# Performance work log

Measured on AMD Instinct MI355X. Metric: run time of the kernel, lower is better.

## Reference

```python
import jax, jax.numpy as jnp
import numpy as np

HEAD_DIM = 128
ROPE_THETA = 10000.0


def _rope_cos_sin(positions, head_dim, theta):
    # positions: [T] int -> cos/sin [T, head_dim] (LLaMA half-split convention)
    inv_freq = 1.0 / (theta ** (jnp.arange(0, head_dim, 2, dtype=jnp.float32) / head_dim))
    ang = positions.astype(jnp.float32)[:, None] * inv_freq  # [T, D/2]
    cos = jnp.concatenate([jnp.cos(ang), jnp.cos(ang)], axis=-1)
    sin = jnp.concatenate([jnp.sin(ang), jnp.sin(ang)], axis=-1)
    return cos, sin


def _apply_rope(x, cos, sin):
    # x: [T, H, D]; rotate_half: (-x2, x1)
    half = x.shape[-1] // 2
    rot = jnp.concatenate([-x[..., half:], x[..., :half]], axis=-1)
    return x * cos[:, None, :] + rot * sin[:, None, :]


def setup_inputs() -> dict:
    key = jax.random.key(0)
    ks = jax.random.split(key, 5)
    T, hid = 4096, 4096
    S = 1024  # equal-length sequences -> B = T // S = 4
    Hq, Hk, D = 32, 8, HEAD_DIM
    hidden = jax.random.normal(ks[0], (T, hid), dtype=jnp.float32)
    positions = (jnp.arange(T, dtype=jnp.int32) % S)
    q_w = jax.random.normal(ks[1], (Hq * D, hid), dtype=jnp.float32) * 0.02
    k_w = jax.random.normal(ks[2], (Hk * D, hid), dtype=jnp.float32) * 0.02
    v_w = jax.random.normal(ks[3], (Hk * D, hid), dtype=jnp.float32) * 0.02
    o_w = jax.random.normal(ks[4], (hid, Hq * D), dtype=jnp.float32) * 0.02
    return {"hidden": hidden, "positions": positions, "q_w": q_w, "k_w": k_w,
            "v_w": v_w, "o_w": o_w, "seq_len": S}


def reference(hidden, positions, q_w, k_w, v_w, o_w, seq_len):
    T, hid = hidden.shape
    D = HEAD_DIM
    Hq = q_w.shape[0] // D
    Hk = k_w.shape[0] // D
    G = Hq // Hk  # num_kv_groups
    S = int(seq_len)
    B = T // S
    # QKV projections (ColumnParallel, tp=1): y = x @ W^T
    q = (hidden @ q_w.T).reshape(T, Hq, D)
    k = (hidden @ k_w.T).reshape(T, Hk, D)
    v = (hidden @ v_w.T).reshape(T, Hk, D)
    # fused RoPE on q and k
    cos, sin = _rope_cos_sin(positions, D, ROPE_THETA)
    q = _apply_rope(q, cos, sin)
    k = _apply_rope(k, cos, sin)
    # varlen (equal-length) causal GQA attention
    q = q.reshape(B, S, Hk, G, D)
    k = k.reshape(B, S, Hk, D)
    v = v.reshape(B, S, Hk, D)
    scale = 1.0 / np.sqrt(D).astype(np.float32)
    scores = jnp.einsum('bqhgd,bkhd->bhgqk', q, k) * scale  # [B,Hk,G,S,S]
    causal = jnp.tril(jnp.ones((S, S), dtype=bool))
    scores = jnp.where(causal, scores, jnp.asarray(-1e30, scores.dtype))
    attn = jax.nn.softmax(scores, axis=-1)
    out = jnp.einsum('bhgqk,bkhd->bqhgd', attn, v).reshape(T, Hq * D)
    # output projection (RowParallel, tp=1)
    return out @ o_w.T
```

## Files before the change

kernel.cpp:

```cpp
#include <hip/hip_runtime.h>
#include <hip/hip_bf16.h>

typedef __attribute__((ext_vector_type(8))) short bf16x8;
typedef __attribute__((ext_vector_type(4))) float f32x4;
typedef __attribute__((ext_vector_type(8))) unsigned short u16x8;

__device__ inline unsigned short f2bf(float f) {
  unsigned u = __builtin_bit_cast(unsigned, f);
  u += 0x7FFFu + ((u >> 16) & 1u);
  return (unsigned short)(u >> 16);
}
__device__ inline float b2f(unsigned short h) {
  unsigned u = ((unsigned)h) << 16;
  return __builtin_bit_cast(float, u);
}

typedef const __attribute__((address_space(1))) void* gas_ptr;
typedef __attribute__((address_space(3))) void* las_ptr;
__device__ inline void load_lds16(const void* g, void* l) {
  __builtin_amdgcn_global_load_lds((gas_ptr)g, (las_ptr)l, 16, 0, 0);
}

#define PHB() do { asm volatile("" ::: "memory"); __builtin_amdgcn_s_barrier(); \
                   __builtin_amdgcn_sched_barrier(0); } while (0)
#define PHB_MID() do { asm volatile("" ::: "memory"); __builtin_amdgcn_s_barrier(); } while (0)

__global__ __launch_bounds__(256) void cvt_f32_bf16(const float* __restrict__ src,
                                                    unsigned short* __restrict__ dst,
                                                    int n4) {
  int i = blockIdx.x * 256 + threadIdx.x;
  if (i >= n4) return;
  float4 v = ((const float4*)src)[i];
  ushort4 o;
  o.x = f2bf(v.x); o.y = f2bf(v.y); o.z = f2bf(v.z); o.w = f2bf(v.w);
  ((ushort4*)dst)[i] = o;
}

__device__ inline void stage_half(const unsigned short* __restrict__ g, int ld,
                                  size_t grow0, int kcol0, char* ldsdst, int tid) {
#pragma unroll
  for (int i = 0; i < 2; ++i) {
    int c = tid + i * 512;
    int r = c >> 3;
    int k = (c & 7) ^ (r & 7);
    load_lds16(g + (grow0 + r) * ld + kcol0 + k * 8, ldsdst + c * 16);
  }
}

template <bool OUT_F32>
__global__ __launch_bounds__(512, 2) void gemm8(const unsigned short* __restrict__ A,
                                                const unsigned short* __restrict__ B,
                                                void* __restrict__ Cv,
                                                int M, int N, int K) {
  __shared__ __attribute__((aligned(16))) char lds[131072];
  const int tid = threadIdx.x;
  const int wave = tid >> 6, lane = tid & 63;
  const int l15 = lane & 15, l4 = lane >> 4, swz = l15 & 7;
  const int wr = wave >> 2, wc = wave & 3;
  const int nTN = N >> 8;
  const int cpx = gridDim.x >> 3;
  const int orig = blockIdx.x;
  const int wg = (orig & 7) * cpx + (orig >> 3);
  const int bm = wg / nTN, bn = wg % nTN;
  const size_t rowA0 = (size_t)bm << 8, rowB0 = (size_t)bn << 8;
  const int nt = K >> 6;
  const int brow = (wc & 1) * 64;

  stage_half(A, K, rowA0,       0,  lds + 0,             tid);
  stage_half(A, K, rowA0 + 128, 0,  lds + 16384,         tid);
  stage_half(B, K, rowB0,       0,  lds + 32768,         tid);
  stage_half(B, K, rowB0 + 128, 0,  lds + 49152,         tid);
  stage_half(A, K, rowA0,       64, lds + 65536,         tid);
  stage_half(A, K, rowA0 + 128, 64, lds + 65536 + 16384, tid);
  stage_half(B, K, rowB0,       64, lds + 65536 + 32768, tid);
  stage_half(B, K, rowB0 + 128, 64, lds + 65536 + 49152, tid);
  asm volatile("s_waitcnt vmcnt(8)" ::: "memory");
  __builtin_amdgcn_s_barrier();
  __builtin_amdgcn_sched_barrier(0);

  f32x4 acc[8][4] = {};
  bf16x8 bf01[2][2];

  {
    const char* bufB0 = lds + 32768 + (wc >> 1) * 16384;
#pragma unroll
    for (int n = 0; n < 2; ++n)
#pragma unroll
      for (int kk = 0; kk < 2; ++kk)
        bf01[n][kk] = *(const bf16x8*)(bufB0 + ((brow + n * 16 + l15) << 7) + (((kk * 4 + l4) ^ swz) << 4));
  }

#pragma unroll 2
  for (int t = 0; t < nt; ++t) {
    char* cbuf = lds + (t & 1) * 65536;
    char* obuf = lds + ((t + 1) & 1) * 65536;
    const char* bufA = cbuf + wr * 16384;
    const char* bufB = cbuf + 32768 + (wc >> 1) * 16384;
    const int kc2 = (t + 2) << 6;

    bf16x8 af[8][2], bf23[2][2];

#pragma unroll
    for (int m = 0; m < 4; ++m)
#pragma unroll
      for (int kk = 0; kk < 2; ++kk)
        af[m][kk] = *(const bf16x8*)(bufA + ((m * 16 + l15) << 7) + (((kk * 4 + l4) ^ swz) << 4));
    PHB_MID();
    __builtin_amdgcn_s_setprio(1);
#pragma unroll
    for (int m = 0; m < 4; ++m)
#pragma unroll
      for (int n = 0; n < 2; ++n)
#pragma unroll
        for (int kk = 0; kk < 2; ++kk)
          acc[m][n] = __builtin_amdgcn_mfma_f32_16x16x32_bf16(af[m][kk], bf01[n][kk], acc[m][n], 0, 0, 0);
    __builtin_amdgcn_s_setprio(0);
    PHB();

#pragma unroll
    for (int n = 0; n < 2; ++n)
#pragma unroll
      for (int kk = 0; kk < 2; ++kk)
        bf23[n][kk] = *(const bf16x8*)(bufB + ((brow + (n + 2) * 16 + l15) << 7) + (((kk * 4 + l4) ^ swz) << 4));
    PHB_MID();
    __builtin_amdgcn_s_setprio(1);
#pragma unroll
    for (int m = 0; m < 4; ++m)
#pragma unroll
      for (int n = 0; n < 2; ++n)
#pragma unroll
        for (int kk = 0; kk < 2; ++kk)
          acc[m][n + 2] = __builtin_amdgcn_mfma_f32_16x16x32_bf16(af[m][kk], bf23[n][kk], acc[m][n + 2], 0, 0, 0);
    __builtin_amdgcn_s_setprio(0);
    PHB();

#pragma unroll
    for (int m = 4; m < 8; ++m)
#pragma unroll
      for (int kk = 0; kk < 2; ++kk)
        af[m][kk] = *(const bf16x8*)(bufA + ((m * 16 + l15) << 7) + (((kk * 4 + l4) ^ swz) << 4));
    if (t < nt - 2) {
      stage_half(B, K, rowB0,       kc2, cbuf + 32768, tid);
      stage_half(B, K, rowB0 + 128, kc2, cbuf + 49152, tid);
    }
    PHB_MID();
    __builtin_amdgcn_s_setprio(1);
#pragma unroll
    for (int m = 4; m < 8; ++m)
#pragma unroll
      for (int n = 0; n < 2; ++n)
#pragma unroll
        for (int kk = 0; kk < 2; ++kk)
          acc[m][n] = __builtin_amdgcn_mfma_f32_16x16x32_bf16(af[m][kk], bf01[n][kk], acc[m][n], 0, 0, 0);
    __builtin_amdgcn_s_setprio(0);
    PHB();

    if (t < nt - 2) {
      stage_half(A, K, rowA0,       kc2, cbuf,         tid);
      stage_half(A, K, rowA0 + 128, kc2, cbuf + 16384, tid);
    }
    if (t <= nt - 3) { asm volatile("s_waitcnt vmcnt(8)" ::: "memory"); }
    else             { asm volatile("s_waitcnt vmcnt(0)" ::: "memory"); }
    PHB_MID();
    if (t < nt - 1) {
      const char* bufB1 = obuf + 32768 + (wc >> 1) * 16384;
#pragma unroll
      for (int n = 0; n < 2; ++n)
#pragma unroll
        for (int kk = 0; kk < 2; ++kk)
          bf01[n][kk] = *(const bf16x8*)(bufB1 + ((brow + n * 16 + l15) << 7) + (((kk * 4 + l4) ^ swz) << 4));
    }
    __builtin_amdgcn_s_setprio(1);
#pragma unroll
    for (int m = 4; m < 8; ++m)
#pragma unroll
      for (int n = 0; n < 2; ++n)
#pragma unroll
        for (int kk = 0; kk < 2; ++kk)
          acc[m][n + 2] = __builtin_amdgcn_mfma_f32_16x16x32_bf16(af[m][kk], bf23[n][kk], acc[m][n + 2], 0, 0, 0);
    __builtin_amdgcn_s_setprio(0);
    PHB();
  }

#pragma unroll
  for (int m = 0; m < 8; ++m)
#pragma unroll
    for (int n = 0; n < 4; ++n)
#pragma unroll
      for (int r = 0; r < 4; ++r) {
        size_t row = rowA0 + wr * 128 + m * 16 + l4 * 4 + r;
        size_t col = rowB0 + wc * 64 + n * 16 + l15;
        float v = acc[m][n][r];
        if (OUT_F32) ((float*)Cv)[row * N + col] = v;
        else         ((unsigned short*)Cv)[row * N + col] = f2bf(v);
      }
}

__global__ __launch_bounds__(256) void rope_kernel(unsigned short* __restrict__ qkv,
                                                   const int* __restrict__ positions) {
  int gw = (blockIdx.x * 256 + threadIdx.x) >> 6;
  int lane = threadIdx.x & 63;
  int t = gw / 40, h = gw % 40;
  size_t col0 = (h < 32) ? ((size_t)h << 7) : (4096 + ((size_t)(h - 32) << 7));
  unsigned short* p = qkv + (size_t)t * 6144 + col0;
  float pos = (float)positions[t];
  float inv = powf(10000.0f, -(float)lane * (1.0f / 64.0f));
  float ang = pos * inv;
  float s, c;
  sincosf(ang, &s, &c);
  float x1 = b2f(p[lane]);
  float x2 = b2f(p[lane + 64]);
  p[lane]      = f2bf(x1 * c - x2 * s);
  p[lane + 64] = f2bf(x2 * c + x1 * s);
}

__global__ __launch_bounds__(256, 4) void attn_kernel(const unsigned short* __restrict__ qkv,
                                                      unsigned short* __restrict__ ao) {
  int orig = blockIdx.x;
  int wgid = (orig & 7) * 128 + (orig >> 3);
  int pair = wgid & 7;
  int hq = (wgid >> 3) & 31;
  int b  = wgid >> 8;
  int hk = hq >> 2;
  int tid = threadIdx.x, wave = tid >> 6, lane = tid & 63;
  int l15 = lane & 15, l4 = lane >> 4;

  __shared__ __attribute__((aligned(16))) char ldsA[16384];
  __shared__ __attribute__((aligned(16))) unsigned short Vt[128][72];
  unsigned short (*Ks)[128]    = (unsigned short (*)[128])ldsA;
  unsigned short (*Ps)[16][72] = (unsigned short (*)[16][72])ldsA;

  const float scale = 0.08838834764831845f;

#pragma unroll 1
  for (int iq = 0; iq < 2; ++iq) {
    const int qa = iq ? (15 - pair) : pair;
    const size_t qrow0 = (size_t)(b * 1024 + qa * 64 + wave * 16);

    bf16x8 qf[4];
    {
      const unsigned short* qp = qkv + (qrow0 + l15) * 6144 + ((size_t)hq << 7) + l4 * 8;
#pragma unroll
      for (int kc = 0; kc < 4; ++kc) qf[kc] = *(const bf16x8*)(qp + kc * 32);
    }

    float m_i[4], l_i[4];
    f32x4 oacc[8];
#pragma unroll
    for (int r = 0; r < 4; ++r) { m_i[r] = -1e30f; l_i[r] = 0.0f; }
#pragma unroll
    for (int d = 0; d < 8; ++d) oacc[d] = f32x4{0.f, 0.f, 0.f, 0.f};

#pragma unroll 1
    for (int kt = 0; kt <= qa; ++kt) {
      __syncthreads();

      const unsigned short* kbase = qkv + (size_t)(b * 1024 + kt * 64) * 6144 + 4096 + ((size_t)hk << 7);
#pragma unroll
      for (int j = 0; j < 4; ++j) {
        int c = (j * 4 + wave) * 64 + lane;
        int r = c >> 4;
        int cc = (c & 15) ^ (r & 7);
        load_lds16(kbase + (size_t)r * 6144 + cc * 8, ldsA + c * 16);
      }
      {
        const unsigned short* vp = qkv + (size_t)(b * 1024 + kt * 64 + lane) * 6144 + 5120 + ((size_t)hk << 7) + wave * 32;
        u16x8 va0 = *(const u16x8*)(vp);
        u16x8 va1 = *(const u16x8*)(vp + 8);
        u16x8 va2 = *(const u16x8*)(vp + 16);
        u16x8 va3 = *(const u16x8*)(vp + 24);
        int d0 = wave * 32;
#pragma unroll
        for (int c = 0; c < 8; ++c) Vt[d0 + c][lane]      = va0[c];
#pragma unroll
        for (int c = 0; c < 8; ++c) Vt[d0 + 8 + c][lane]  = va1[c];
#pragma unroll
        for (int c = 0; c < 8; ++c) Vt[d0 + 16 + c][lane] = va2[c];
#pragma unroll
        for (int c = 0; c < 8; ++c) Vt[d0 + 24 + c][lane] = va3[c];
      }
      __syncthreads();

      float pbuf[4][4];
      float tmax[4] = {-1e30f, -1e30f, -1e30f, -1e30f};
#pragma unroll
      for (int nt = 0; nt < 4; ++nt) {
        f32x4 sacc = {0.f, 0.f, 0.f, 0.f};
        int row = nt * 16 + l15;
#pragma unroll
        for (int kc = 0; kc < 4; ++kc) {
          const unsigned short* kp = &Ks[0][0] + row * 128 + (((kc * 4 + l4) ^ (row & 7)) * 8);
          bf16x8 kf = *(const bf16x8*)kp;
          sacc = __builtin_amdgcn_mfma_f32_16x16x32_bf16(qf[kc], kf, sacc, 0, 0, 0);
        }
#pragma unroll
        for (int r = 0; r < 4; ++r) {
          float s = sacc[r] * scale;
          if (kt == qa) {
            int kcol = nt * 16 + l15;
            int qrow = wave * 16 + l4 * 4 + r;
            if (kcol > qrow) s = -1e30f;
          }
          pbuf[nt][r] = s;
          tmax[r] = fmaxf(tmax[r], s);
        }
      }
      __syncthreads();

#pragma unroll
      for (int r = 0; r < 4; ++r) {
        float v = tmax[r];
        v = fmaxf(v, __shfl_xor(v, 1));
        v = fmaxf(v, __shfl_xor(v, 2));
        v = fmaxf(v, __shfl_xor(v, 4));
        v = fmaxf(v, __shfl_xor(v, 8));
        tmax[r] = v;
      }
      float rescale[4];
#pragma unroll
      for (int r = 0; r < 4; ++r) {
        float mn = fmaxf(m_i[r], tmax[r]);
        rescale[r] = __expf(m_i[r] - mn);
        m_i[r] = mn;
      }
      float psum[4] = {0.f, 0.f, 0.f, 0.f};
#pragma unroll
      for (int nt = 0; nt < 4; ++nt)
#pragma unroll
        for (int r = 0; r < 4; ++r) {
          float p = __expf(pbuf[nt][r] - m_i[r]);
          pbuf[nt][r] = p;
          psum[r] += p;
        }
#pragma unroll
      for (int r = 0; r < 4; ++r) {
        float v = psum[r];
        v += __shfl_xor(v, 1);
        v += __shfl_xor(v, 2);
        v += __shfl_xor(v, 4);
        v += __shfl_xor(v, 8);
        l_i[r] = l_i[r] * rescale[r] + v;
      }
#pragma unroll
      for (int d = 0; d < 8; ++d)
#pragma unroll
        for (int r = 0; r < 4; ++r) oacc[d][r] *= rescale[r];

#pragma unroll
      for (int nt = 0; nt < 4; ++nt)
#pragma unroll
        for (int r = 0; r < 4; ++r)
          Ps[wave][l4 * 4 + r][nt * 16 + l15] = f2bf(pbuf[nt][r]);

#pragma unroll
      for (int h = 0; h < 2; ++h) {
        bf16x8 pa = *(const bf16x8*)&Ps[wave][l15][h * 32 + l4 * 8];
#pragma unroll
        for (int d = 0; d < 8; ++d) {
          bf16x8 vf = *(const bf16x8*)&Vt[d * 16 + l15][h * 32 + l4 * 8];
          oacc[d] = __builtin_amdgcn_mfma_f32_16x16x32_bf16(pa, vf, oacc[d], 0, 0, 0);
        }
      }
    }

#pragma unroll
    for (int d = 0; d < 8; ++d)
#pragma unroll
      for (int r = 0; r < 4; ++r) {
        size_t row = qrow0 + l4 * 4 + r;
        size_t col = ((size_t)hq << 7) + d * 16 + l15;
        ao[row * 4096 + col] = f2bf(oacc[d][r] / l_i[r]);
      }
  }
}

extern "C" void kernel_launch(void* const* d_in, const int* in_sizes, int n_in,
                              void* d_out, int out_size, void* d_ws, size_t ws_size,
                              hipStream_t stream) {
  const float* hidden    = (const float*)d_in[0];
  const int*   positions = (const int*)d_in[1];
  const float* q_w       = (const float*)d_in[2];
  const float* k_w       = (const float*)d_in[3];
  const float* v_w       = (const float*)d_in[4];
  const float* o_w       = (const float*)d_in[5];
  float* out = (float*)d_out;

  char* ws = (char*)d_ws;
  unsigned short* hidB  = (unsigned short*)(ws);
  unsigned short* wqkvB = (unsigned short*)(ws + 33554432);
  unsigned short* woB   = (unsigned short*)(ws + 83886080);
  unsigned short* qkvB  = (unsigned short*)(ws + 117440512);
  unsigned short* aoB   = (unsigned short*)(ws + 167772160);

  cvt_f32_bf16<<<16384, 256, 0, stream>>>(hidden, hidB, 4194304);
  cvt_f32_bf16<<<16384, 256, 0, stream>>>(q_w, wqkvB, 4194304);
  cvt_f32_bf16<<<4096, 256, 0, stream>>>(k_w, wqkvB + 16777216, 1048576);
  cvt_f32_bf16<<<4096, 256, 0, stream>>>(v_w, wqkvB + 20971520, 1048576);
  cvt_f32_bf16<<<16384, 256, 0, stream>>>(o_w, woB, 4194304);

  gemm8<false><<<384, 512, 0, stream>>>(hidB, wqkvB, (void*)qkvB, 4096, 6144, 4096);

  rope_kernel<<<40960, 256, 0, stream>>>(qkvB, positions);

  attn_kernel<<<1024, 256, 0, stream>>>(qkvB, aoB);

  gemm8<true><<<256, 512, 0, stream>>>(aoB, woB, (void*)out, 4096, 4096, 4096);
}
```

Measured before the change: 565.5 us.

## Reorder GEMM MFMA phases with cross-iteration A prefetch and defer V transpose in attention

```diff
diff --git a/kernel.cpp b/kernel.cpp
--- a/kernel.cpp
+++ b/kernel.cpp
@@ -47,42 +47,48 @@
   }
 }
 
-template <bool OUT_F32>
+template <int Kc, int Nc, bool OUT_F32>
 __global__ __launch_bounds__(512, 2) void gemm8(const unsigned short* __restrict__ A,
                                                 const unsigned short* __restrict__ B,
-                                                void* __restrict__ Cv,
-                                                int M, int N, int K) {
+                                                void* __restrict__ Cv) {
   __shared__ __attribute__((aligned(16))) char lds[131072];
   const int tid = threadIdx.x;
   const int wave = tid >> 6, lane = tid & 63;
   const int l15 = lane & 15, l4 = lane >> 4, swz = l15 & 7;
   const int wr = wave >> 2, wc = wave & 3;
-  const int nTN = N >> 8;
+  const int nTN = Nc >> 8;
   const int cpx = gridDim.x >> 3;
   const int orig = blockIdx.x;
   const int wg = (orig & 7) * cpx + (orig >> 3);
   const int bm = wg / nTN, bn = wg % nTN;
   const size_t rowA0 = (size_t)bm << 8, rowB0 = (size_t)bn << 8;
-  const int nt = K >> 6;
+  const int nt = Kc >> 6;
   const int brow = (wc & 1) * 64;
 
-  stage_half(A, K, rowA0,       0,  lds + 0,             tid);
-  stage_half(A, K, rowA0 + 128, 0,  lds + 16384,         tid);
-  stage_half(B, K, rowB0,       0,  lds + 32768,         tid);
-  stage_half(B, K, rowB0 + 128, 0,  lds + 49152,         tid);
-  stage_half(A, K, rowA0,       64, lds + 65536,         tid);
-  stage_half(A, K, rowA0 + 128, 64, lds + 65536 + 16384, tid);
-  stage_half(B, K, rowB0,       64, lds + 65536 + 32768, tid);
-  stage_half(B, K, rowB0 + 128, 64, lds + 65536 + 49152, tid);
+  stage_half(A, Kc, rowA0,       0,  lds + 0,             tid);
+  stage_half(A, Kc, rowA0 + 128, 0,  lds + 16384,         tid);
+  stage_half(B, Kc, rowB0,       0,  lds + 32768,         tid);
+  stage_half(B, Kc, rowB0 + 128, 0,  lds + 49152,         tid);
+  stage_half(A, Kc, rowA0,       64, lds + 65536,         tid);
+  stage_half(A, Kc, rowA0 + 128, 64, lds + 65536 + 16384, tid);
+  stage_half(B, Kc, rowB0,       64, lds + 65536 + 32768, tid);
+  stage_half(B, Kc, rowB0 + 128, 64, lds + 65536 + 49152, tid);
   asm volatile("s_waitcnt vmcnt(8)" ::: "memory");
   __builtin_amdgcn_s_barrier();
   __builtin_amdgcn_sched_barrier(0);
 
   f32x4 acc[8][4] = {};
+  bf16x8 af[8][2];
   bf16x8 bf01[2][2];
 
   {
+    const char* bufA0 = lds + wr * 16384;
     const char* bufB0 = lds + 32768 + (wc >> 1) * 16384;
+#pragma unroll
+    for (int m = 0; m < 4; ++m)
+#pragma unroll
+      for (int kk = 0; kk < 2; ++kk)
+        af[m][kk] = *(const bf16x8*)(bufA0 + ((m * 16 + l15) << 7) + (((kk * 4 + l4) ^ swz) << 4));
 #pragma unroll
     for (int n = 0; n < 2; ++n)
 #pragma unroll
@@ -98,10 +104,27 @@
     const char* bufB = cbuf + 32768 + (wc >> 1) * 16384;
     const int kc2 = (t + 2) << 6;
 
-    bf16x8 af[8][2], bf23[2][2];
-
+    bf16x8 bf23[2][2];
+
+#pragma unroll
+    for (int n = 0; n < 2; ++n)
+#pragma unroll
+      for (int kk = 0; kk < 2; ++kk)
+        bf23[n][kk] = *(const bf16x8*)(bufB + ((brow + (n + 2) * 16 + l15) << 7) + (((kk * 4 + l4) ^ swz) << 4));
+    PHB_MID();
+    __builtin_amdgcn_s_setprio(1);
 #pragma unroll
     for (int m = 0; m < 4; ++m)
+#pragma unroll
+      for (int n = 0; n < 2; ++n)
+#pragma unroll
+        for (int kk = 0; kk < 2; ++kk)
+          acc[m][n] = __builtin_amdgcn_mfma_f32_16x16x32_bf16(af[m][kk], bf01[n][kk], acc[m][n], 0, 0, 0);
+    __builtin_amdgcn_s_setprio(0);
+    PHB();
+
+#pragma unroll
+    for (int m = 4; m < 8; ++m)
 #pragma unroll
       for (int kk = 0; kk < 2; ++kk)
         af[m][kk] = *(const bf16x8*)(bufA + ((m * 16 + l15) << 7) + (((kk * 4 + l4) ^ swz) << 4));
@@ -113,62 +136,51 @@
       for (int n = 0; n < 2; ++n)
 #pragma unroll
         for (int kk = 0; kk < 2; ++kk)
+          acc[m][n + 2] = __builtin_amdgcn_mfma_f32_16x16x32_bf16(af[m][kk], bf23[n][kk], acc[m][n + 2], 0, 0, 0);
+    __builtin_amdgcn_s_setprio(0);
+    PHB();
+
+    if (t < nt - 2) {
+      stage_half(B, Kc, rowB0,       kc2, cbuf + 32768, tid);
+      stage_half(B, Kc, rowB0 + 128, kc2, cbuf + 49152, tid);
+    }
+    PHB_MID();
+    __builtin_amdgcn_s_setprio(1);
+#pragma unroll
+    for (int m = 4; m < 8; ++m)
+#pragma unroll
+      for (int n = 0; n < 2; ++n)
+#pragma unroll
+        for (int kk = 0; kk < 2; ++kk)
           acc[m][n] = __builtin_amdgcn_mfma_f32_16x16x32_bf16(af[m][kk], bf01[n][kk], acc[m][n], 0, 0, 0);
     __builtin_amdgcn_s_setprio(0);
     PHB();
 
-#pragma unroll
-    for (int n = 0; n < 2; ++n)
-#pragma unroll
-      for (int kk = 0; kk < 2; ++kk)
-        bf23[n][kk] = *(const bf16x8*)(bufB + ((brow + (n + 2) * 16 + l15) << 7) + (((kk * 4 + l4) ^ swz) << 4));
-    PHB_MID();
-    __builtin_amdgcn_s_setprio(1);
-#pragma unroll
-    for (int m = 0; m < 4; ++m)
-#pragma unroll
-      for (int n = 0; n < 2; ++n)
-#pragma unroll
-        for (int kk = 0; kk < 2; ++kk)
-          acc[m][n + 2] = __builtin_amdgcn_mfma_f32_16x16x32_bf16(af[m][kk], bf23[n][kk], acc[m][n + 2], 0, 0, 0);
-    __builtin_amdgcn_s_setprio(0);
-    PHB();
-
-#pragma unroll
-    for (int m = 4; m < 8; ++m)
-#pragma unroll
-      for (int kk = 0; kk < 2; ++kk)
-        af[m][kk] = *(const bf16x8*)(bufA + ((m * 16 + l15) << 7) + (((kk * 4 + l4) ^ swz) << 4));
     if (t < nt - 2) {
-      stage_half(B, K, rowB0,       kc2, cbuf + 32768, tid);
-      stage_half(B, K, rowB0 + 128, kc2, cbuf + 49152, tid);
-    }
-    PHB_MID();
-    __builtin_amdgcn_s_setprio(1);
-#pragma unroll
-    for (int m = 4; m < 8; ++m)
-#pragma unroll
-      for (int n = 0; n < 2; ++n)
-#pragma unroll
-        for (int kk = 0; kk < 2; ++kk)
-          acc[m][n] = __builtin_amdgcn_mfma_f32_16x16x32_bf16(af[m][kk], bf01[n][kk], acc[m][n], 0, 0, 0);
-    __builtin_amdgcn_s_setprio(0);
-    PHB();
-
-    if (t < nt - 2) {
-      stage_half(A, K, rowA0,       kc2, cbuf,         tid);
-      stage_half(A, K, rowA0 + 128, kc2, cbuf + 16384, tid);
+      stage_half(A, Kc, rowA0,       kc2, cbuf,         tid);
+      stage_half(A, Kc, rowA0 + 128, kc2, cbuf + 16384, tid);
     }
     if (t <= nt - 3) { asm volatile("s_waitcnt vmcnt(8)" ::: "memory"); }
     else             { asm volatile("s_waitcnt vmcnt(0)" ::: "memory"); }
     PHB_MID();
     if (t < nt - 1) {
+      const char* bufA1 = obuf + wr * 16384;
       const char* bufB1 = obuf + 32768 + (wc >> 1) * 16384;
 #pragma unroll
+      for (int m = 0; m < 2; ++m)
+#pragma unroll
+        for (int kk = 0; kk < 2; ++kk)
+          af[m][kk] = *(const bf16x8*)(bufA1 + ((m * 16 + l15) << 7) + (((kk * 4 + l4) ^ swz) << 4));
+#pragma unroll
       for (int n = 0; n < 2; ++n)
 #pragma unroll
         for (int kk = 0; kk < 2; ++kk)
           bf01[n][kk] = *(const bf16x8*)(bufB1 + ((brow + n * 16 + l15) << 7) + (((kk * 4 + l4) ^ swz) << 4));
+#pragma unroll
+      for (int m = 2; m < 4; ++m)
+#pragma unroll
+        for (int kk = 0; kk < 2; ++kk)
+          af[m][kk] = *(const bf16x8*)(bufA1 + ((m * 16 + l15) << 7) + (((kk * 4 + l4) ^ swz) << 4));
     }
     __builtin_amdgcn_s_setprio(1);
 #pragma unroll
@@ -191,8 +203,8 @@
         size_t row = rowA0 + wr * 128 + m * 16 + l4 * 4 + r;
         size_t col = rowB0 + wc * 64 + n * 16 + l15;
         float v = acc[m][n][r];
-        if (OUT_F32) ((float*)Cv)[row * N + col] = v;
-        else         ((unsigned short*)Cv)[row * N + col] = f2bf(v);
+        if (OUT_F32) ((float*)Cv)[row * Nc + col] = v;
+        else         ((unsigned short*)Cv)[row * Nc + col] = f2bf(v);
       }
 }
 
@@ -263,23 +275,14 @@
         int cc = (c & 15) ^ (r & 7);
         load_lds16(kbase + (size_t)r * 6144 + cc * 8, ldsA + c * 16);
       }
-      {
-        const unsigned short* vp = qkv + (size_t)(b * 1024 + kt * 64 + lane) * 6144 + 5120 + ((size_t)hk << 7) + wave * 32;
-        u16x8 va0 = *(const u16x8*)(vp);
-        u16x8 va1 = *(const u16x8*)(vp + 8);
-        u16x8 va2 = *(const u16x8*)(vp + 16);
-        u16x8 va3 = *(const u16x8*)(vp + 24);
-        int d0 = wave * 32;
-#pragma unroll
-        for (int c = 0; c < 8; ++c) Vt[d0 + c][lane]      = va0[c];
-#pragma unroll
-        for (int c = 0; c < 8; ++c) Vt[d0 + 8 + c][lane]  = va1[c];
-#pragma unroll
-        for (int c = 0; c < 8; ++c) Vt[d0 + 16 + c][lane] = va2[c];
-#pragma unroll
-        for (int c = 0; c < 8; ++c) Vt[d0 + 24 + c][lane] = va3[c];
-      }
-      __syncthreads();
+      const unsigned short* vp = qkv + (size_t)(b * 1024 + kt * 64 + lane) * 6144 + 5120 + ((size_t)hk << 7) + wave * 32;
+      u16x8 va0 = *(const u16x8*)(vp);
+      u16x8 va1 = *(const u16x8*)(vp + 8);
+      u16x8 va2 = *(const u16x8*)(vp + 16);
+      u16x8 va3 = *(const u16x8*)(vp + 24);
+      asm volatile("s_waitcnt vmcnt(4)" ::: "memory");
+      __builtin_amdgcn_s_barrier();
+      __builtin_amdgcn_sched_barrier(0);
 
       float pbuf[4][4];
       float tmax[4] = {-1e30f, -1e30f, -1e30f, -1e30f};
@@ -305,7 +308,9 @@
           tmax[r] = fmaxf(tmax[r], s);
         }
       }
-      __syncthreads();
+      asm volatile("" ::: "memory");
+      __builtin_amdgcn_s_barrier();
+      __builtin_amdgcn_sched_barrier(0);
 
 #pragma unroll
       for (int r = 0; r < 4; ++r) {
@@ -351,6 +356,21 @@
 #pragma unroll
         for (int r = 0; r < 4; ++r)
           Ps[wave][l4 * 4 + r][nt * 16 + l15] = f2bf(pbuf[nt][r]);
+
+      {
+        int d0 = wave * 32;
+#pragma unroll
+        for (int c = 0; c < 8; ++c) Vt[d0 + c][lane]      = va0[c];
+#pragma unroll
+        for (int c = 0; c < 8; ++c) Vt[d0 + 8 + c][lane]  = va1[c];
+#pragma unroll
+        for (int c = 0; c < 8; ++c) Vt[d0 + 16 + c][lane] = va2[c];
+#pragma unroll
+        for (int c = 0; c < 8; ++c) Vt[d0 + 24 + c][lane] = va3[c];
+      }
+      asm volatile("s_waitcnt lgkmcnt(0)" ::: "memory");
+      __builtin_amdgcn_s_barrier();
+      __builtin_amdgcn_sched_barrier(0);
 
 #pragma unroll
       for (int h = 0; h < 2; ++h) {
@@ -398,11 +418,11 @@
   cvt_f32_bf16<<<4096, 256, 0, stream>>>(v_w, wqkvB + 20971520, 1048576);
   cvt_f32_bf16<<<16384, 256, 0, stream>>>(o_w, woB, 4194304);
 
-  gemm8<false><<<384, 512, 0, stream>>>(hidB, wqkvB, (void*)qkvB, 4096, 6144, 4096);
+  gemm8<4096, 6144, false><<<384, 512, 0, stream>>>(hidB, wqkvB, (void*)qkvB);
 
   rope_kernel<<<40960, 256, 0, stream>>>(qkvB, positions);
 
   attn_kernel<<<1024, 256, 0, stream>>>(qkvB, aoB);
 
-  gemm8<true><<<256, 512, 0, stream>>>(aoB, woB, (void*)out, 4096, 4096, 4096);
-}
+  gemm8<4096, 4096, true><<<256, 512, 0, stream>>>(aoB, woB, (void*)out);
+}
```

Measured after the change: 599.5 us. 6.0% more time.
